# Kernel tuning notes

Measured on AMD Instinct MI355X. Metric: run time of the kernel, lower is better.

The kernel has to match this reference:

```python
import jax, jax.numpy as jnp
import numpy as np

B, SEQ, PRED, DM = 16, 2048, 2048, 64
P = SEQ + PRED            # PointNum = 4096, per-node feature length
NLAYER, HID = 3, 4096     # MLPNums, ggdmodel hidden sizes
NH, HS = 16, 4096         # NumAttentionHeads, HiddenSize
G_CONST, K = 1.0, 8
NN = DM * DM              # 4096 == P, MHSA input dim (required by original code)


def setup_inputs() -> dict:
    key = jax.random.key(0)
    ks = jax.random.split(key, 11)
    s_mlp = 1.0 / np.sqrt(P).astype(np.float32)
    s_att = 1.0 / np.sqrt(NN).astype(np.float32)
    s_out = 1.0 / np.sqrt(HS).astype(np.float32)
    return {
        "x": jax.random.normal(ks[0], (B, P, DM), jnp.float32),
        "W_mlp": jax.random.normal(ks[1], (NLAYER, P, HID), jnp.float32) * s_mlp,
        "b_mlp": jnp.zeros((NLAYER, HID), jnp.float32),
        "Wq": jax.random.normal(ks[2], (NN, HS), jnp.float32) * s_att,
        "bq": jnp.zeros((HS,), jnp.float32),
        "Wk": jax.random.normal(ks[3], (NN, HS), jnp.float32) * s_att,
        "bk": jnp.zeros((HS,), jnp.float32),
        "Wv": jax.random.normal(ks[4], (NN, HS), jnp.float32) * s_att,
        "bv": jnp.zeros((HS,), jnp.float32),
        "Wo": jax.random.normal(ks[5], (HS, HS), jnp.float32) * s_out,
        "bo": jnp.zeros((HS,), jnp.float32),
    }


def _grav_adj(h):
    # h: [B, N, D] node features -> symmetrized, top-K masked gravity adjacency [B, N, N]
    norm = jnp.linalg.norm(h, axis=-1)                      # [B, N]
    m = jnp.sum(h, axis=-1) / norm                          # node "mass"
    sim = jnp.einsum('bnd,bmd->bnm', h, h) / (norm[:, :, None] * norm[:, None, :])
    F = G_CONST * m[:, :, None] * m[:, None, :] * sim * sim  # gravity matrix
    kth = jax.lax.top_k(F, K)[0][..., -1:]                  # per-row Kth largest value
    F = jnp.where(F >= kth, F, 0.0)                         # keep only top-K per row
    F = jnp.maximum(F, 0.0)                                 # ReLU
    return 0.5 * (F + jnp.swapaxes(F, -1, -2))              # symmetrize


def reference(x, W_mlp, b_mlp, Wq, bq, Wk, bk, Wv, bv, Wo, bo):
    h = jnp.swapaxes(x, 1, 2)                               # [B, N=DM, P]
    adjs = [_grav_adj(h)]
    for l in range(NLAYER):                                 # each MLP applied to the same h
        hv = h @ W_mlp[l] + b_mlp[l]                        # [B, N, HID]
        adjs.append(_grav_adj(hv))
    A = jnp.stack(adjs, axis=1)                             # [B, L, N, N], L = NLAYER + 1
    Lseq = A.shape[1]
    tok = A.reshape(B, Lseq, NN)                            # L tokens of dim N*N
    dh = HS // NH
    q = (tok @ Wq + bq).reshape(B, Lseq, NH, dh)
    k = (tok @ Wk + bk).reshape(B, Lseq, NH, dh)
    v = (tok @ Wv + bv).reshape(B, Lseq, NH, dh)
    scores = jnp.einsum('blhd,bmhd->bhlm', q, k) / np.sqrt(dh).astype(np.float32)
    attn = jax.nn.softmax(scores, axis=-1)
    ctx = jnp.einsum('bhlm,bmhd->blhd', attn, v).reshape(B, Lseq, HS)
    out = ctx @ Wo + bo                                     # [B, L, HS]
    return jnp.where(out > 0.5, out, 0.0)
```

## Files before the change

### kernel.cpp

```cpp
#include <hip/hip_runtime.h>
#include <math.h>


#define B16 16
#define PDIM 4096
#define NNODE 64
#define NCHUNK 32
#define KCG 128

typedef __attribute__((ext_vector_type(8))) short bf16x8;
typedef __attribute__((ext_vector_type(4))) float f32x4;
typedef __attribute__((ext_vector_type(4))) unsigned short us4;
typedef __attribute__((ext_vector_type(8))) unsigned short us8;

__device__ inline void split2(float x, unsigned short& h, unsigned short& l) {
  unsigned u = __float_as_uint(x);
  unsigned hu = (u + 0x7fffu + ((u >> 16) & 1u)) & 0xffff0000u;
  h = (unsigned short)(hu >> 16);
  float lo = x - __uint_as_float(hu);
  unsigned u2 = __float_as_uint(lo);
  l = (unsigned short)((u2 + 0x7fffu + ((u2 >> 16) & 1u)) >> 16);
}

__device__ inline void gload16(const void* g, void* lds) {
  __builtin_amdgcn_global_load_lds((const unsigned int*)g, (unsigned int*)lds, 16, 0, 0);
}

__global__ __launch_bounds__(256) void k_transpose(const float* __restrict__ x,
                                                   float* __restrict__ h,
                                                   unsigned short* __restrict__ AhT,
                                                   unsigned short* __restrict__ AlT,
                                                   int mode) {
  __shared__ float t[64][65];
  int b = blockIdx.y;
  int p0 = blockIdx.x * 64;
  const float* xb = x + (size_t)b * PDIM * NNODE;
#pragma unroll
  for (int i = 0; i < 16; ++i) {
    int e = i * 256 + threadIdx.x;
    int p = e >> 6, n = e & 63;
    t[p][n] = xb[(size_t)p0 * 64 + e];
  }
  __syncthreads();
  if (mode != 2) {
    float* hb = h + (size_t)b * NNODE * PDIM;
#pragma unroll
    for (int i = 0; i < 16; ++i) {
      int e = i * 256 + threadIdx.x;
      int n = e >> 6, p = e & 63;
      hb[(size_t)n * PDIM + p0 + p] = t[p][n];
    }
  }
  if (mode == 0) return;
#pragma unroll
  for (int j = 0; j < 2; ++j) {
    int cid = j * 256 + threadIdx.x;
    int n2 = cid >> 3, kg8 = cid & 7;
    us8 hv_, lv_;
#pragma unroll
    for (int e = 0; e < 8; ++e) {
      unsigned short hh, ll;
      split2(t[kg8 * 8 + e][n2], hh, ll);
      hv_[e] = hh; lv_[e] = ll;
    }
    int m = b * 64 + n2;
    int ks = (p0 >> 5) + (kg8 >> 2);
    size_t idx = (((size_t)(m >> 7) * 128 + ks) * 8 + ((m >> 4) & 7)) * 512 +
                 (size_t)((n2 & 15) + 16 * (kg8 & 3)) * 8;
    *(us8*)&AhT[idx] = hv_;
    *(us8*)&AlT[idx] = lv_;
  }
}

__global__ __launch_bounds__(256) void k_wsplit(const float* __restrict__ W,
                                                unsigned short* __restrict__ WhT,
                                                unsigned short* __restrict__ WlT) {
  __shared__ float Wt[32][132];
  int nb = blockIdx.x, kb = blockIdx.y;
  int tid = threadIdx.x;
#pragma unroll
  for (int i = 0; i < 4; ++i) {
    int idx = i * 256 + tid;
    int row = idx >> 5, c4 = idx & 31;
    float4 v = *(const float4*)&W[(size_t)(kb * 32 + row) * 4096 + nb * 128 + c4 * 4];
    *(float4*)&Wt[row][c4 * 4] = v;
  }
  __syncthreads();
#pragma unroll
  for (int j = 0; j < 2; ++j) {
    int cid = j * 256 + tid;
    int nl = cid & 127, kg = cid >> 7;
    us8 hv_, lv_;
#pragma unroll
    for (int e = 0; e < 8; ++e) {
      unsigned short hh, ll;
      split2(Wt[kg * 8 + e][nl], hh, ll);
      hv_[e] = hh; lv_[e] = ll;
    }
    size_t idx = (((size_t)nb * 128 + kb) * 8 + (nl >> 4)) * 512 +
                 (size_t)((nl & 15) + 16 * kg) * 8;
    *(us8*)&WhT[idx] = hv_;
    *(us8*)&WlT[idx] = lv_;
  }
}

__global__ __launch_bounds__(1024) void k_gemm_mlp(
    const unsigned short* __restrict__ Ah, const unsigned short* __restrict__ Al,
    const unsigned short* __restrict__ Bh, const unsigned short* __restrict__ Bl,
    float* __restrict__ Cp) {
  __shared__ unsigned short sAh[2][8192], sAl[2][8192];
  __shared__ unsigned short sBh[2][8192], sBl[2][8192];
  int tid = threadIdx.x;
  int l = tid & 63, wid = tid >> 6;
  int wr = wid >> 2, wc = wid & 3;
  int nb = blockIdx.x, mb = blockIdx.y, z = blockIdx.z;
  const int spp = 32;
  int ks0 = z * spp;

  int half = tid >> 9, off8 = (tid & 511) * 8;
  size_t gA = (size_t)(mb * 2 + half) * 128;
  size_t gB = (size_t)(nb * 2 + half) * 128;

  f32x4 acc[4][4];
#pragma unroll
  for (int i = 0; i < 4; ++i)
#pragma unroll
    for (int j = 0; j < 4; ++j) acc[i][j] = (f32x4){0.f, 0.f, 0.f, 0.f};

  gload16(Ah + (gA + ks0) * 4096 + off8, &sAh[0][tid * 8]);
  gload16(Al + (gA + ks0) * 4096 + off8, &sAl[0][tid * 8]);
  gload16(Bh + (gB + ks0) * 4096 + off8, &sBh[0][tid * 8]);
  gload16(Bl + (gB + ks0) * 4096 + off8, &sBl[0][tid * 8]);
  __syncthreads();

  int buf = 0;
  for (int t = 0; t < spp; ++t) {
    if (t + 1 < spp) {
      size_t ks = ks0 + t + 1;
      gload16(Ah + (gA + ks) * 4096 + off8, &sAh[buf ^ 1][tid * 8]);
      gload16(Al + (gA + ks) * 4096 + off8, &sAl[buf ^ 1][tid * 8]);
      gload16(Bh + (gB + ks) * 4096 + off8, &sBh[buf ^ 1][tid * 8]);
      gload16(Bl + (gB + ks) * 4096 + off8, &sBl[buf ^ 1][tid * 8]);
    }
    bf16x8 ah[4], al4[4], bh4[4], bl4[4];
#pragma unroll
    for (int i = 0; i < 4; ++i) {
      ah[i]  = *(const bf16x8*)&sAh[buf][(wr * 4 + i) * 512 + l * 8];
      al4[i] = *(const bf16x8*)&sAl[buf][(wr * 4 + i) * 512 + l * 8];
      bh4[i] = *(const bf16x8*)&sBh[buf][(wc * 4 + i) * 512 + l * 8];
      bl4[i] = *(const bf16x8*)&sBl[buf][(wc * 4 + i) * 512 + l * 8];
    }
#pragma unroll
    for (int mt = 0; mt < 4; ++mt)
#pragma unroll
      for (int nt = 0; nt < 4; ++nt) {
        acc[mt][nt] = __builtin_amdgcn_mfma_f32_16x16x32_bf16(ah[mt],  bh4[nt], acc[mt][nt], 0, 0, 0);
        acc[mt][nt] = __builtin_amdgcn_mfma_f32_16x16x32_bf16(ah[mt],  bl4[nt], acc[mt][nt], 0, 0, 0);
        acc[mt][nt] = __builtin_amdgcn_mfma_f32_16x16x32_bf16(al4[mt], bh4[nt], acc[mt][nt], 0, 0, 0);
      }
    __syncthreads();
    buf ^= 1;
  }

  int n0 = nb * 256, m0 = mb * 256;
  float* Cz = Cp + (size_t)z * (1024 * 4096);
#pragma unroll
  for (int mt = 0; mt < 4; ++mt)
#pragma unroll
    for (int nt = 0; nt < 4; ++nt) {
      int col = n0 + wc * 64 + nt * 16 + (l & 15);
      int rowb = m0 + wr * 64 + mt * 16 + ((l >> 4) << 2);
#pragma unroll
      for (int r = 0; r < 4; ++r)
        Cz[(size_t)(rowb + r) * 4096 + col] = acc[mt][nt][r];
    }
}

__global__ __launch_bounds__(512) void k_gemm_wsf32(
    const unsigned short* __restrict__ Ah, const unsigned short* __restrict__ Al,
    const float* __restrict__ W0, const float* __restrict__ W1,
    const float* __restrict__ W2, float* __restrict__ Cp, int ksplit) {
  __shared__ unsigned short sAh[2][2048], sAl[2][2048];
  __shared__ unsigned short sBh[2][4096], sBl[2][4096];
  int tid = threadIdx.x;
  int l = tid & 63, wid = tid >> 6;
  int wr = wid >> 2, wc = wid & 3;
  int nb = blockIdx.x, z = blockIdx.z;
  int mat = z / ksplit, kz = z - mat * ksplit;
  const float* W = (mat == 0) ? W0 : ((mat == 1) ? W1 : W2);
  int nsteps = 128 / ksplit;
  int ks0 = kz * nsteps;
  int n0 = nb * 128;

  const float* wbase = W + (size_t)((l >> 4) * 8) * 4096 + n0 + wid * 16 + (l & 15);
  int sidx = wid * 512 + l * 8;

  f32x4 acc[2][2];
#pragma unroll
  for (int i = 0; i < 2; ++i)
#pragma unroll
    for (int j = 0; j < 2; ++j) acc[i][j] = (f32x4){0.f, 0.f, 0.f, 0.f};

  {
    if (tid < 256) gload16(Ah + (size_t)ks0 * 4096 + tid * 8, &sAh[0][tid * 8]);
    else           gload16(Al + (size_t)ks0 * 4096 + (tid - 256) * 8, &sAl[0][(tid - 256) * 8]);
    float wv[8];
#pragma unroll
    for (int e = 0; e < 8; ++e) wv[e] = wbase[(size_t)ks0 * 131072 + (size_t)e * 4096];
    us8 hi, lo;
#pragma unroll
    for (int e = 0; e < 8; ++e) {
      unsigned short hh, ll;
      split2(wv[e], hh, ll);
      hi[e] = hh; lo[e] = ll;
    }
    *(us8*)&sBh[0][sidx] = hi;
    *(us8*)&sBl[0][sidx] = lo;
  }
  __syncthreads();

  int buf = 0;
  for (int t = 0; t < nsteps; ++t) {
    bool more = (t + 1 < nsteps);
    float wv[8];
    if (more) {
      int ks = ks0 + t + 1;
      if (tid < 256) gload16(Ah + (size_t)ks * 4096 + tid * 8, &sAh[buf ^ 1][tid * 8]);
      else           gload16(Al + (size_t)ks * 4096 + (tid - 256) * 8, &sAl[buf ^ 1][(tid - 256) * 8]);
#pragma unroll
      for (int e = 0; e < 8; ++e) wv[e] = wbase[(size_t)ks * 131072 + (size_t)e * 4096];
    }
    bf16x8 aH[2], aL[2], bH[2], bL[2];
#pragma unroll
    for (int i = 0; i < 2; ++i) {
      aH[i] = *(const bf16x8*)&sAh[buf][(wr * 2 + i) * 512 + l * 8];
      aL[i] = *(const bf16x8*)&sAl[buf][(wr * 2 + i) * 512 + l * 8];
      bH[i] = *(const bf16x8*)&sBh[buf][(wc * 2 + i) * 512 + l * 8];
      bL[i] = *(const bf16x8*)&sBl[buf][(wc * 2 + i) * 512 + l * 8];
    }
#pragma unroll
    for (int i = 0; i < 2; ++i)
#pragma unroll
      for (int j = 0; j < 2; ++j) {
        acc[i][j] = __builtin_amdgcn_mfma_f32_16x16x32_bf16(aH[i], bH[j], acc[i][j], 0, 0, 0);
        acc[i][j] = __builtin_amdgcn_mfma_f32_16x16x32_bf16(aH[i], bL[j], acc[i][j], 0, 0, 0);
        acc[i][j] = __builtin_amdgcn_mfma_f32_16x16x32_bf16(aL[i], bH[j], acc[i][j], 0, 0, 0);
      }
    if (more) {
      us8 hi, lo;
#pragma unroll
      for (int e = 0; e < 8; ++e) {
        unsigned short hh, ll;
        split2(wv[e], hh, ll);
        hi[e] = hh; lo[e] = ll;
      }
      *(us8*)&sBh[buf ^ 1][sidx] = hi;
      *(us8*)&sBl[buf ^ 1][sidx] = lo;
    }
    __syncthreads();
    buf ^= 1;
  }

  float* Cz = Cp + (size_t)z * 262144;
#pragma unroll
  for (int i = 0; i < 2; ++i)
#pragma unroll
    for (int j = 0; j < 2; ++j) {
      int col = n0 + wc * 32 + j * 16 + (l & 15);
#pragma unroll
      for (int r = 0; r < 4; ++r) {
        int row = (wr * 2 + i) * 16 + ((l >> 4) << 2) + r;
        Cz[(size_t)row * 4096 + col] = acc[i][j][r];
      }
    }
}

__global__ __launch_bounds__(256) void k_red_mlp_split(const float* __restrict__ Cp,
                                                       const float* __restrict__ bias,
                                                       unsigned short* __restrict__ hvh,
                                                       unsigned short* __restrict__ hvl) {
  int c = blockIdx.x * 256 + threadIdx.x;
  int m = c >> 9, kc = c & 511;
  int k0 = kc * 8;
  const float* p = Cp + (size_t)m * 4096 + k0;
  us8 hv_, lv_;
#pragma unroll
  for (int e = 0; e < 8; ++e) {
    float v = p[e] + p[e + 4194304] + p[e + 2 * 4194304] + p[e + 3 * 4194304] + bias[k0 + e];
    unsigned short hh, ll;
    split2(v, hh, ll);
    hv_[e] = hh; lv_[e] = ll;
  }
  int batch = m >> 6, rr = m & 63;
  size_t idx = (size_t)batch * 262144 + (size_t)(kc >> 2) * 2048 +
               (size_t)(rr >> 4) * 512 + (size_t)((rr & 15) + 16 * (kc & 3)) * 8;
  *(us8*)&hvh[idx] = hv_;
  *(us8*)&hvl[idx] = lv_;
}

__global__ __launch_bounds__(256) void k_gram_mfma(
    const unsigned short* __restrict__ Zh, const unsigned short* __restrict__ Zl,
    float* __restrict__ Gp, float* __restrict__ Sp,
    int bs1, int ks_stride, int nsteps) {
  __shared__ unsigned short sZh[2][2048], sZl[2][2048];
  int z = blockIdx.x, b = blockIdx.y;
  int tid = threadIdx.x;
  int l = tid & 63, w = tid >> 6;
  size_t zbase = (size_t)(b >> 1) * 524288 + (size_t)(b & 1) * bs1;
  int ks0 = z * nsteps;

  f32x4 acc[4], racc;
#pragma unroll
  for (int j = 0; j < 4; ++j) acc[j] = (f32x4){0.f, 0.f, 0.f, 0.f};
  racc = (f32x4){0.f, 0.f, 0.f, 0.f};
  bf16x8 ones;
#pragma unroll
  for (int e = 0; e < 8; ++e) ones[e] = (short)0x3F80;

  gload16(Zh + zbase + (size_t)ks0 * ks_stride + tid * 8, &sZh[0][tid * 8]);
  gload16(Zl + zbase + (size_t)ks0 * ks_stride + tid * 8, &sZl[0][tid * 8]);
  __syncthreads();

  int buf = 0;
  for (int t = 0; t < nsteps; ++t) {
    if (t + 1 < nsteps) {
      size_t off = zbase + (size_t)(ks0 + t + 1) * ks_stride + tid * 8;
      gload16(Zh + off, &sZh[buf ^ 1][tid * 8]);
      gload16(Zl + off, &sZl[buf ^ 1][tid * 8]);
    }
    bf16x8 bh[4], bl4[4];
#pragma unroll
    for (int nt = 0; nt < 4; ++nt) {
      bh[nt]  = *(const bf16x8*)&sZh[buf][nt * 512 + l * 8];
      bl4[nt] = *(const bf16x8*)&sZl[buf][nt * 512 + l * 8];
    }
    bf16x8 ah = bh[w], al = bl4[w];
#pragma unroll
    for (int nt = 0; nt < 4; ++nt) {
      acc[nt] = __builtin_amdgcn_mfma_f32_16x16x32_bf16(ah, bh[nt], acc[nt], 0, 0, 0);
      acc[nt] = __builtin_amdgcn_mfma_f32_16x16x32_bf16(ah, bl4[nt], acc[nt], 0, 0, 0);
      acc[nt] = __builtin_amdgcn_mfma_f32_16x16x32_bf16(al, bh[nt], acc[nt], 0, 0, 0);
    }
    racc = __builtin_amdgcn_mfma_f32_16x16x32_bf16(ah, ones, racc, 0, 0, 0);
    racc = __builtin_amdgcn_mfma_f32_16x16x32_bf16(al, ones, racc, 0, 0, 0);
    __syncthreads();
    buf ^= 1;
  }

  float* Gz = Gp + ((size_t)z * B16 + b) * 4096;
#pragma unroll
  for (int nt = 0; nt < 4; ++nt) {
    int col = nt * 16 + (l & 15);
#pragma unroll
    for (int r = 0; r < 4; ++r) {
      int row = w * 16 + ((l >> 4) << 2) + r;
      Gz[row * 64 + col] = acc[nt][r];
    }
  }
  if ((l & 15) == 0) {
    float* Sz = Sp + ((size_t)z * B16 + b) * 64;
#pragma unroll
    for (int r = 0; r < 4; ++r) Sz[w * 16 + ((l >> 4) << 2) + r] = racc[r];
  }
}

__global__ __launch_bounds__(256) void k_gred8(const float* __restrict__ Gp,
                                               const float* __restrict__ Sp,
                                               float* __restrict__ G,
                                               float* __restrict__ S, int slot) {
  int idx = blockIdx.x * 256 + threadIdx.x;
  if (idx < 65536) {
    float s = 0.f;
#pragma unroll
    for (int c = 0; c < 8; ++c) s += Gp[(size_t)c * 65536 + idx];
    G[(size_t)slot * 65536 + idx] = s;
  } else if (idx < 66560) {
    int i2 = idx - 65536;
    float s = 0.f;
#pragma unroll
    for (int c = 0; c < 8; ++c) s += Sp[(size_t)c * 1024 + i2];
    S[(size_t)slot * 1024 + i2] = s;
  }
}

__global__ __launch_bounds__(256) void k_redqkv8(const float* __restrict__ Cp,
                                                 const float* __restrict__ bq,
                                                 const float* __restrict__ bk,
                                                 const float* __restrict__ bv,
                                                 float* __restrict__ q,
                                                 float* __restrict__ k,
                                                 float* __restrict__ v) {
  int idx = blockIdx.x * 256 + threadIdx.x;
  int mat = idx >> 18;
  int rn = idx & ((1 << 18) - 1);
  int n = rn & 4095;
  const float* base = Cp + (size_t)mat * 8 * 262144;
  float s = 0.f;
#pragma unroll
  for (int p = 0; p < 8; ++p) s += base[(size_t)p * 262144 + rn];
  if (mat == 0) q[rn] = s + bq[n];
  else if (mat == 1) k[rn] = s + bk[n];
  else v[rn] = s + bv[n];
}

__global__ __launch_bounds__(256) void k_redN(const float* __restrict__ Cp,
                                              const float* __restrict__ bias,
                                              float* __restrict__ dst,
                                              int nparts, int thr) {
  int idx = blockIdx.x * 256 + threadIdx.x;
  float s = bias[idx & 4095];
  for (int p = 0; p < nparts; ++p) s += Cp[(size_t)p * 262144 + idx];
  if (thr) s = (s > 0.5f) ? s : 0.f;
  dst[idx] = s;
}

__device__ inline float wmax64(float v) {
#pragma unroll
  for (int off = 32; off; off >>= 1) v = fmaxf(v, __shfl_xor(v, off));
  return v;
}

__global__ __launch_bounds__(256) void k_adj_t(const float* __restrict__ G,
                                               const float* __restrict__ S,
                                               unsigned short* __restrict__ tokh,
                                               unsigned short* __restrict__ tokl) {
  __shared__ float Fm[64][64];
  __shared__ float nrm[64], mm[64];
  int b = blockIdx.x >> 2, lz = blockIdx.x & 3;
  int tid = threadIdx.x;
  int j = tid & 63, w = tid >> 6;
  const float* Gb = G + ((size_t)lz * B16 + b) * 4096;
  const float* Sb = S + ((size_t)lz * B16 + b) * 64;
  if (tid < 64) {
    float nj = sqrtf(Gb[tid * 64 + tid]);
    nrm[tid] = nj;
    mm[tid] = Sb[tid] / nj;
  }
  __syncthreads();
  for (int i = w; i < 64; i += 4) {
    float g = Gb[i * 64 + j];
    float sim = g / (nrm[i] * nrm[j]);
    Fm[i][j] = mm[i] * mm[j] * sim * sim;
  }
  __syncthreads();
  for (int i = w; i < 64; i += 4) {
    float f = Fm[i][j];
    int cnt = 0;
#pragma unroll
    for (int u4 = 0; u4 < 16; ++u4) {
      float4 q = *(const float4*)&Fm[i][u4 * 4];
      cnt += (q.x > f) + (q.y > f) + (q.z > f) + (q.w > f);
    }
    float cand = (cnt <= 7) ? f : INFINITY;
#pragma unroll
    for (int off = 32; off; off >>= 1) cand = fminf(cand, __shfl_xor(cand, off));
    float fm = (f >= cand) ? fmaxf(f, 0.f) : 0.f;
    Fm[i][j] = fm;
  }
  __syncthreads();
  int r = b * 4 + lz;
  int mt = r >> 4, rl = r & 15;
#pragma unroll
  for (int c = 0; c < 2; ++c) {
    int cid = tid * 2 + c;
    int jj0 = cid >> 3, g = cid & 7;
    us8 hv_, lv_;
#pragma unroll
    for (int e = 0; e < 8; ++e) {
      int kcol = g * 8 + e;
      float val = 0.5f * (Fm[jj0][kcol] + Fm[kcol][jj0]);
      unsigned short hh, ll;
      split2(val, hh, ll);
      hv_[e] = hh; lv_[e] = ll;
    }
    int ks = jj0 * 2 + (g >> 2);
    size_t idx = ((size_t)ks * 8 + mt) * 512 + (size_t)(rl + 16 * (g & 3)) * 8;
    *(us8*)&tokh[idx] = hv_;
    *(us8*)&tokl[idx] = lv_;
  }
}

__global__ __launch_bounds__(64) void k_attn_t(const float* __restrict__ q,
                                               const float* __restrict__ k,
                                               const float* __restrict__ v,
                                               unsigned short* __restrict__ ctxh,
                                               unsigned short* __restrict__ ctxl) {
  __shared__ float cb[4][256];
  int hd = blockIdx.x, b = blockIdx.y;
  int t = threadIdx.x;
  float qr[4][4], kr[4][4], vr[4][4];
#pragma unroll
  for (int l = 0; l < 4; ++l)
#pragma unroll
    for (int s = 0; s < 4; ++s) {
      size_t off = ((size_t)(b * 4 + l)) * 4096 + hd * 256 + t + s * 64;
      qr[l][s] = q[off]; kr[l][s] = k[off]; vr[l][s] = v[off];
    }
  float sc[4][4];
#pragma unroll
  for (int l = 0; l < 4; ++l)
#pragma unroll
    for (int m = 0; m < 4; ++m) {
      float p = 0.f;
#pragma unroll
      for (int s = 0; s < 4; ++s) p = fmaf(qr[l][s], kr[m][s], p);
#pragma unroll
      for (int off = 32; off; off >>= 1) p += __shfl_xor(p, off);
      sc[l][m] = p * (1.0f / 16.0f);
    }
  float at[4][4];
#pragma unroll
  for (int l = 0; l < 4; ++l) {
    float mx = fmaxf(fmaxf(sc[l][0], sc[l][1]), fmaxf(sc[l][2], sc[l][3]));
    float e0 = expf(sc[l][0] - mx), e1 = expf(sc[l][1] - mx);
    float e2 = expf(sc[l][2] - mx), e3 = expf(sc[l][3] - mx);
    float d = e0 + e1 + e2 + e3;
    at[l][0] = e0 / d; at[l][1] = e1 / d; at[l][2] = e2 / d; at[l][3] = e3 / d;
  }
#pragma unroll
  for (int l = 0; l < 4; ++l)
#pragma unroll
    for (int s = 0; s < 4; ++s) {
      float c = 0.f;
#pragma unroll
      for (int m = 0; m < 4; ++m) c = fmaf(at[l][m], vr[m][s], c);
      cb[l][s * 64 + t] = c;
    }
  __syncthreads();
  int lq = t >> 4, c16 = t & 15;
  int mt = b >> 2, rl = (b & 3) * 4 + lq;
#pragma unroll
  for (int e8 = 0; e8 < 2; ++e8) {
    us8 hv_, lv_;
#pragma unroll
    for (int e = 0; e < 8; ++e) {
      unsigned short hh, ll;
      split2(cb[lq][c16 * 16 + e8 * 8 + e], hh, ll);
      hv_[e] = hh; lv_[e] = ll;
    }
    int ks = hd * 8 + (c16 >> 1);
    size_t idx = ((size_t)ks * 8 + mt) * 512 + (size_t)(rl + 16 * ((c16 * 2 + e8) & 3)) * 8;
    *(us8*)&ctxh[idx] = hv_;
    *(us8*)&ctxl[idx] = lv_;
  }
}

__global__ __launch_bounds__(256) void k_gram_partial(const float* __restrict__ Z,
                                                      float* __restrict__ Gp,
                                                      float* __restrict__ Sp) {
  __shared__ float Zt[KCG][68];
  int c = blockIdx.x, b = blockIdx.y;
  int tid = threadIdx.x;
  const float* Zb = Z + (size_t)b * NNODE * PDIM + c * KCG;
#pragma unroll
  for (int i = 0; i < 32; ++i) {
    int e = i * 256 + tid;
    int r = e >> 7, kk = e & 127;
    Zt[kk][r] = Zb[(size_t)r * PDIM + kk];
  }
  __syncthreads();
  int ii = tid >> 2, j0 = (tid & 3) << 4;
  float acc[16] = {};
  for (int kk = 0; kk < KCG; ++kk) {
    float zi = Zt[kk][ii];
    float4 z0 = *(const float4*)&Zt[kk][j0 + 0];
    float4 z1 = *(const float4*)&Zt[kk][j0 + 4];
    float4 z2 = *(const float4*)&Zt[kk][j0 + 8];
    float4 z3 = *(const float4*)&Zt[kk][j0 + 12];
    acc[0] = fmaf(zi, z0.x, acc[0]);   acc[1] = fmaf(zi, z0.y, acc[1]);
    acc[2] = fmaf(zi, z0.z, acc[2]);   acc[3] = fmaf(zi, z0.w, acc[3]);
    acc[4] = fmaf(zi, z1.x, acc[4]);   acc[5] = fmaf(zi, z1.y, acc[5]);
    acc[6] = fmaf(zi, z1.z, acc[6]);   acc[7] = fmaf(zi, z1.w, acc[7]);
    acc[8] = fmaf(zi, z2.x, acc[8]);   acc[9] = fmaf(zi, z2.y, acc[9]);
    acc[10] = fmaf(zi, z2.z, acc[10]); acc[11] = fmaf(zi, z2.w, acc[11]);
    acc[12] = fmaf(zi, z3.x, acc[12]); acc[13] = fmaf(zi, z3.y, acc[13]);
    acc[14] = fmaf(zi, z3.z, acc[14]); acc[15] = fmaf(zi, z3.w, acc[15]);
  }
  float* gp = Gp + ((size_t)c * B16 + b) * 4096 + ii * 64 + j0;
#pragma unroll
  for (int j = 0; j < 16; ++j) gp[j] = acc[j];
  if (tid < 64) {
    float s = 0.f;
    for (int kk = 0; kk < KCG; ++kk) s += Zt[kk][tid];
    Sp[((size_t)c * B16 + b) * 64 + tid] = s;
  }
}

__global__ __launch_bounds__(256) void k_gram_reduce(const float* __restrict__ Gp,
                                                     const float* __restrict__ Sp,
                                                     float* __restrict__ G,
                                                     float* __restrict__ S, int slot) {
  int idx = blockIdx.x * 256 + threadIdx.x;
  if (idx < B16 * 4096) {
    float s = 0.f;
    for (int c = 0; c < NCHUNK; ++c) s += Gp[(size_t)c * (B16 * 4096) + idx];
    G[(size_t)slot * (B16 * 4096) + idx] = s;
  } else {
    int idx2 = idx - B16 * 4096;
    float s = 0.f;
    for (int c = 0; c < NCHUNK; ++c) s += Sp[(size_t)c * (B16 * 64) + idx2];
    S[(size_t)slot * (B16 * 64) + idx2] = s;
  }
}

__global__ __launch_bounds__(256) void k_gemm_mfma(
    const float* __restrict__ A, const float* __restrict__ B0,
    const float* __restrict__ B1, const float* __restrict__ B2,
    const float* __restrict__ bias, float* __restrict__ C,
    int mrows, int mstore, int N, int K, int ksplit) {
  __shared__ __align__(16) unsigned short sA[2][8][64][8];
  __shared__ __align__(16) unsigned short sB[2][8][64][8];
  int z = blockIdx.z;
  int mat = z / ksplit, ks = z - mat * ksplit;
  const float* Bm = (mat == 0) ? B0 : ((mat == 1) ? B1 : B2);
  int kchunk = K / ksplit;
  int k0 = ks * kchunk, k1 = k0 + kchunk;
  int tid = threadIdx.x;
  int l = tid & 63;
  int wr = (tid >> 7) & 1, wc = (tid >> 6) & 1;
  int m0 = blockIdx.y * 128, n0g = blockIdx.x * 128;
  bool activeM = (m0 + wr * 64) < mstore;
  int am = tid >> 1;
  int arow = m0 + am; if (arow >= mrows) arow = mrows - 1;
  const float* Arow = A + (size_t)arow * K;
  int amt = am >> 4;
  int bk = tid >> 3;
  int bnb = (tid & 7) * 4;
  int bg = bk >> 3, bslot = bk & 7;
  f32x4 acc[4][4];
#pragma unroll
  for (int i = 0; i < 4; ++i)
#pragma unroll
    for (int j = 0; j < 4; ++j) acc[i][j] = (f32x4){0.f, 0.f, 0.f, 0.f};
  for (int kb = k0; kb < k1; kb += 32) {
    __syncthreads();
#pragma unroll
    for (int i = 0; i < 4; ++i) {
      int kq = (tid & 1) * 4 + i * 8;
      float4 a = *(const float4*)(Arow + kb + kq);
      unsigned short h0, h1, h2, h3, l0, l1, l2, l3;
      split2(a.x, h0, l0); split2(a.y, h1, l1);
      split2(a.z, h2, l2); split2(a.w, h3, l3);
      int lane_t = (am & 15) + 16 * (kq >> 3);
      int sb = kq & 4;
      *(us4*)&sA[0][amt][lane_t][sb] = (us4){h0, h1, h2, h3};
      *(us4*)&sA[1][amt][lane_t][sb] = (us4){l0, l1, l2, l3};
    }
    {
      const float* Brow = Bm + (size_t)(kb + bk) * N + n0g;
#pragma unroll
      for (int i = 0; i < 4; ++i) {
        int n = bnb + i * 32;
        int nt = n >> 4, nr = n & 15;
        float4 b = *(const float4*)(Brow + n);
        float be[4] = {b.x, b.y, b.z, b.w};
#pragma unroll
        for (int e = 0; e < 4; ++e) {
          unsigned short hh, ll;
          split2(be[e], hh, ll);
          sB[0][nt][nr + e + 16 * bg][bslot] = hh;
          sB[1][nt][nr + e + 16 * bg][bslot] = ll;
        }
      }
    }
    __syncthreads();
    if (!activeM) continue;
    bf16x8 ah[4], al[4], bh[4], bl[4];
#pragma unroll
    for (int t = 0; t < 4; ++t) {
      ah[t] = *(const bf16x8*)&sA[0][wr * 4 + t][l][0];
      al[t] = *(const bf16x8*)&sA[1][wr * 4 + t][l][0];
      bh[t] = *(const bf16x8*)&sB[0][wc * 4 + t][l][0];
      bl[t] = *(const bf16x8*)&sB[1][wc * 4 + t][l][0];
    }
#pragma unroll
    for (int mt = 0; mt < 4; ++mt)
#pragma unroll
      for (int nt = 0; nt < 4; ++nt) {
        acc[mt][nt] = __builtin_amdgcn_mfma_f32_16x16x32_bf16(ah[mt], bh[nt], acc[mt][nt], 0, 0, 0);
        acc[mt][nt] = __builtin_amdgcn_mfma_f32_16x16x32_bf16(ah[mt], bl[nt], acc[mt][nt], 0, 0, 0);
        acc[mt][nt] = __builtin_amdgcn_mfma_f32_16x16x32_bf16(al[mt], bh[nt], acc[mt][nt], 0, 0, 0);
      }
  }
  if (!activeM) return;
  float* Cz = C + (size_t)z * mstore * N;
#pragma unroll
  for (int mt = 0; mt < 4; ++mt)
#pragma unroll
    for (int nt = 0; nt < 4; ++nt) {
      int col = n0g + wc * 64 + nt * 16 + (l & 15);
      float badd = bias ? bias[col] : 0.f;
#pragma unroll
      for (int r = 0; r < 4; ++r) {
        int row = m0 + wr * 64 + mt * 16 + ((l >> 4) << 2) + r;
        if (row < mstore) Cz[(size_t)row * N + col] = acc[mt][nt][r] + badd;
      }
    }
}

__global__ __launch_bounds__(64) void k_adj_fb(const float* __restrict__ G,
                                               const float* __restrict__ S,
                                               float* __restrict__ tok) {
  __shared__ float Fm[64][64];
  __shared__ float nrm[64], mm[64];
  int b = blockIdx.x >> 2, lz = blockIdx.x & 3;
  int j = threadIdx.x;
  const float* Gb = G + ((size_t)lz * B16 + b) * 4096;
  const float* Sb = S + ((size_t)lz * B16 + b) * 64;
  float nj = sqrtf(Gb[j * 64 + j]);
  nrm[j] = nj;
  mm[j] = Sb[j] / nj;
  __syncthreads();
  for (int i = 0; i < 64; ++i) {
    float g = Gb[i * 64 + j];
    float sim = g / (nrm[i] * nj);
    float F = mm[i] * mm[j] * sim * sim;
    float v = F;
    bool act = true;
    float kth = 0.f;
#pragma unroll
    for (int it = 0; it < 8; ++it) {
      float mv = wmax64(act ? v : -INFINITY);
      kth = mv;
      unsigned long long ball = __ballot(act && (v == mv));
      int first = __ffsll(ball) - 1;
      if (j == first) act = false;
    }
    float fm = (F >= kth) ? F : 0.f;
    Fm[i][j] = fmaxf(fm, 0.f);
  }
  __syncthreads();
  float* tb = tok + ((size_t)b * 4 + lz) * 4096;
  for (int i = 0; i < 64; ++i) tb[i * 64 + j] = 0.5f * (Fm[i][j] + Fm[j][i]);
}

__global__ __launch_bounds__(256) void k_qkv_reduce(const float* __restrict__ Cp,
                                                    const float* __restrict__ bq,
                                                    const float* __restrict__ bk,
                                                    const float* __restrict__ bv,
                                                    float* __restrict__ q,
                                                    float* __restrict__ k,
                                                    float* __restrict__ v) {
  int idx = blockIdx.x * 256 + threadIdx.x;
  int mat = idx >> 18;
  int rn = idx & ((1 << 18) - 1);
  int n = rn & 4095;
  const float* base = Cp + (size_t)mat * 4 * 262144;
  float s = base[rn] + base[rn + 262144] + base[rn + 2 * 262144] + base[rn + 3 * 262144];
  if (mat == 0) q[rn] = s + bq[n];
  else if (mat == 1) k[rn] = s + bk[n];
  else v[rn] = s + bv[n];
}

__global__ __launch_bounds__(64) void k_attn_fb(const float* __restrict__ q,
                                                const float* __restrict__ k,
                                                const float* __restrict__ v,
                                                float* __restrict__ ctx) {
  int hd = blockIdx.x, b = blockIdx.y;
  int t = threadIdx.x;
  float qr[4][4], kr[4][4], vr[4][4];
#pragma unroll
  for (int l = 0; l < 4; ++l)
#pragma unroll
    for (int s = 0; s < 4; ++s) {
      size_t off = ((size_t)(b * 4 + l)) * 4096 + hd * 256 + t + s * 64;
      qr[l][s] = q[off]; kr[l][s] = k[off]; vr[l][s] = v[off];
    }
  float sc[4][4];
#pragma unroll
  for (int l = 0; l < 4; ++l)
#pragma unroll
    for (int m = 0; m < 4; ++m) {
      float p = 0.f;
#pragma unroll
      for (int s = 0; s < 4; ++s) p = fmaf(qr[l][s], kr[m][s], p);
#pragma unroll
      for (int off = 32; off; off >>= 1) p += __shfl_xor(p, off);
      sc[l][m] = p * (1.0f / 16.0f);
    }
  float at[4][4];
#pragma unroll
  for (int l = 0; l < 4; ++l) {
    float mx = fmaxf(fmaxf(sc[l][0], sc[l][1]), fmaxf(sc[l][2], sc[l][3]));
    float e0 = expf(sc[l][0] - mx), e1 = expf(sc[l][1] - mx);
    float e2 = expf(sc[l][2] - mx), e3 = expf(sc[l][3] - mx);
    float d = e0 + e1 + e2 + e3;
    at[l][0] = e0 / d; at[l][1] = e1 / d; at[l][2] = e2 / d; at[l][3] = e3 / d;
  }
#pragma unroll
  for (int l = 0; l < 4; ++l)
#pragma unroll
    for (int s = 0; s < 4; ++s) {
      float c = 0.f;
#pragma unroll
      for (int m = 0; m < 4; ++m) c = fmaf(at[l][m], vr[m][s], c);
      ctx[((size_t)(b * 4 + l)) * 4096 + hd * 256 + t + s * 64] = c;
    }
}

__global__ __launch_bounds__(256) void k_out_reduce(const float* __restrict__ Cp,
                                                    const float* __restrict__ bo,
                                                    float* __restrict__ out) {
  int idx = blockIdx.x * 256 + threadIdx.x;
  int n = idx & 4095;
  float s = bo[n];
#pragma unroll
  for (int p = 0; p < 8; ++p) s += Cp[(size_t)p * 262144 + idx];
  out[idx] = (s > 0.5f) ? s : 0.f;
}

extern "C" void kernel_launch(void* const* d_in, const int* in_sizes, int n_in,
                              void* d_out, int out_size, void* d_ws, size_t ws_size,
                              hipStream_t stream) {
  const float* x     = (const float*)d_in[0];
  const float* W_mlp = (const float*)d_in[1];
  const float* b_mlp = (const float*)d_in[2];
  const float* Wq = (const float*)d_in[3]; const float* bq = (const float*)d_in[4];
  const float* Wk = (const float*)d_in[5]; const float* bk = (const float*)d_in[6];
  const float* Wv = (const float*)d_in[7]; const float* bv = (const float*)d_in[8];
  const float* Wo = (const float*)d_in[9]; const float* bo = (const float*)d_in[10];
  float* out = (float*)d_out;
  float* ws = (float*)d_ws;

  float* h   = ws;
  float* Gp  = ws + 8388608;
  float* Sp  = ws + 10485760;
  float* G   = ws + 10518528;
  float* S   = ws + 10780672;

  const size_t NEED = 50368512ull * 4ull;
  if (ws_size >= NEED) {
    unsigned short* hvh = (unsigned short*)(ws + 4194304);
    unsigned short* hvl = (unsigned short*)(ws + 6291456);
    float* q   = ws + 10784768;
    float* kk  = ws + 11046912;
    float* vv  = ws + 11309056;
    unsigned short* AhT = (unsigned short*)(ws + 11571200);
    unsigned short* AlT = (unsigned short*)(ws + 13668352);
    unsigned short* WhT = (unsigned short*)(ws + 15765504);
    unsigned short* WlT = (unsigned short*)(ws + 24154112);
    float* Cp           = ws + 32542720;
    unsigned short* tokh = (unsigned short*)(ws + 49319936);
    unsigned short* tokl = (unsigned short*)(ws + 49582080);
    unsigned short* ctxh = (unsigned short*)(ws + 49844224);
    unsigned short* ctxl = (unsigned short*)(ws + 50106368);

    k_transpose<<<dim3(64, 16), 256, 0, stream>>>(x, h, AhT, AlT, 2);

    k_gram_mfma<<<dim3(8, 16), 256, 0, stream>>>(AhT, AlT, Gp, Sp, 2048, 4096, 16);
    k_gred8<<<260, 256, 0, stream>>>(Gp, Sp, G, S, 0);

    for (int l = 0; l < 3; ++l) {
      k_wsplit<<<dim3(32, 128), 256, 0, stream>>>(W_mlp + (size_t)l * 16777216, WhT, WlT);
      k_gemm_mlp<<<dim3(16, 4, 4), 1024, 0, stream>>>(AhT, AlT, WhT, WlT, Cp);
      k_red_mlp_split<<<2048, 256, 0, stream>>>(Cp, b_mlp + (size_t)l * 4096, hvh, hvl);
      k_gram_mfma<<<dim3(8, 16), 256, 0, stream>>>(hvh, hvl, Gp, Sp, 262144, 2048, 16);
      k_gred8<<<260, 256, 0, stream>>>(Gp, Sp, G, S, l + 1);
    }

    k_adj_t<<<64, 256, 0, stream>>>(G, S, tokh, tokl);

    k_gemm_wsf32<<<dim3(32, 1, 24), 512, 0, stream>>>(tokh, tokl, Wq, Wk, Wv, Cp, 8);
    k_redqkv8<<<3072, 256, 0, stream>>>(Cp, bq, bk, bv, q, kk, vv);

    k_attn_t<<<dim3(16, 16), 64, 0, stream>>>(q, kk, vv, ctxh, ctxl);

    k_gemm_wsf32<<<dim3(32, 1, 8), 512, 0, stream>>>(ctxh, ctxl, Wo, Wo, Wo, Cp, 8);
    k_redN<<<1024, 256, 0, stream>>>(Cp, bo, out, 8, 1);
  } else {
    float* hv  = ws + 4194304;
    float* tok = ws + 10784768;
    float* q   = ws + 11046912;
    float* kk  = ws + 11309056;
    float* vv  = ws + 11571200;
    float* ctx = ws + 11833344;
    float* qkvp = hv;
    float* op   = h;

    k_transpose<<<dim3(64, 16), 256, 0, stream>>>(x, h, (unsigned short*)0,
                                                  (unsigned short*)0, 0);
    k_gram_partial<<<dim3(NCHUNK, 16), 256, 0, stream>>>(h, Gp, Sp);
    k_gram_reduce<<<260, 256, 0, stream>>>(Gp, Sp, G, S, 0);
    for (int l = 0; l < 3; ++l) {
      const float* Wl = W_mlp + (size_t)l * PDIM * 4096;
      const float* bl = b_mlp + (size_t)l * 4096;
      k_gemm_mfma<<<dim3(32, 8, 1), 256, 0, stream>>>(h, Wl, Wl, Wl, bl, hv,
                                                      1024, 1024, 4096, 4096, 1);
      k_gram_partial<<<dim3(NCHUNK, 16), 256, 0, stream>>>(hv, Gp, Sp);
      k_gram_reduce<<<260, 256, 0, stream>>>(Gp, Sp, G, S, l + 1);
    }
    k_adj_fb<<<64, 64, 0, stream>>>(G, S, tok);
    k_gemm_mfma<<<dim3(32, 1, 12), 256, 0, stream>>>(tok, Wq, Wk, Wv, nullptr, qkvp,
                                                     64, 64, 4096, 4096, 4);
    k_qkv_reduce<<<3072, 256, 0, stream>>>(qkvp, bq, bk, bv, q, kk, vv);
    k_attn_fb<<<dim3(16, 16), 64, 0, stream>>>(q, kk, vv, ctx);
    k_gemm_mfma<<<dim3(32, 1, 8), 256, 0, stream>>>(ctx, Wo, Wo, Wo, nullptr, op,
                                                    64, 64, 4096, 4096, 8);
    k_out_reduce<<<1024, 256, 0, stream>>>(op, bo, out);
  }
}
```

Measured before the change: 654.8 us.

## Prefetch two stages ahead in split-bf16 GEMM with fine-grained vmcnt waits

Restructures the double-buffered LDS pipeline of the split-bf16 GEMM. Both buffers are now loaded up front, and each iteration issues the load for stage t+2 after the compute barrier. Explicit s_waitcnt vmcnt(4) plus raw s_barrier replace __syncthreads, so one stage of async global-to-LDS loads stays in flight during the MFMA work. This is meant to hide global load latency better. It relies on the direct-to-LDS loads being counted by vmcnt and correctly ordered, and any mistake there risks a race.

```diff
diff --git a/kernel.cpp b/kernel.cpp
--- a/kernel.cpp
+++ b/kernel.cpp
@@ -127,21 +127,22 @@
 #pragma unroll
     for (int j = 0; j < 4; ++j) acc[i][j] = (f32x4){0.f, 0.f, 0.f, 0.f};
 
-  gload16(Ah + (gA + ks0) * 4096 + off8, &sAh[0][tid * 8]);
-  gload16(Al + (gA + ks0) * 4096 + off8, &sAl[0][tid * 8]);
-  gload16(Bh + (gB + ks0) * 4096 + off8, &sBh[0][tid * 8]);
-  gload16(Bl + (gB + ks0) * 4096 + off8, &sBl[0][tid * 8]);
-  __syncthreads();
-
-  int buf = 0;
+  gload16(Ah + (gA + ks0 + 0) * 4096 + off8, &sAh[0][tid * 8]);
+  gload16(Al + (gA + ks0 + 0) * 4096 + off8, &sAl[0][tid * 8]);
+  gload16(Bh + (gB + ks0 + 0) * 4096 + off8, &sBh[0][tid * 8]);
+  gload16(Bl + (gB + ks0 + 0) * 4096 + off8, &sBl[0][tid * 8]);
+  gload16(Ah + (gA + ks0 + 1) * 4096 + off8, &sAh[1][tid * 8]);
+  gload16(Al + (gA + ks0 + 1) * 4096 + off8, &sAl[1][tid * 8]);
+  gload16(Bh + (gB + ks0 + 1) * 4096 + off8, &sBh[1][tid * 8]);
+  gload16(Bl + (gB + ks0 + 1) * 4096 + off8, &sBl[1][tid * 8]);
+
   for (int t = 0; t < spp; ++t) {
-    if (t + 1 < spp) {
-      size_t ks = ks0 + t + 1;
-      gload16(Ah + (gA + ks) * 4096 + off8, &sAh[buf ^ 1][tid * 8]);
-      gload16(Al + (gA + ks) * 4096 + off8, &sAl[buf ^ 1][tid * 8]);
-      gload16(Bh + (gB + ks) * 4096 + off8, &sBh[buf ^ 1][tid * 8]);
-      gload16(Bl + (gB + ks) * 4096 + off8, &sBl[buf ^ 1][tid * 8]);
-    }
+    int buf = t & 1;
+    if (t + 1 < spp) asm volatile("s_waitcnt vmcnt(4)" ::: "memory");
+    else             asm volatile("s_waitcnt vmcnt(0)" ::: "memory");
+    __builtin_amdgcn_s_barrier();
+    asm volatile("" ::: "memory");
+
     bf16x8 ah[4], al4[4], bh4[4], bl4[4];
 #pragma unroll
     for (int i = 0; i < 4; ++i) {
@@ -158,8 +159,17 @@
         acc[mt][nt] = __builtin_amdgcn_mfma_f32_16x16x32_bf16(ah[mt],  bl4[nt], acc[mt][nt], 0, 0, 0);
         acc[mt][nt] = __builtin_amdgcn_mfma_f32_16x16x32_bf16(al4[mt], bh4[nt], acc[mt][nt], 0, 0, 0);
       }
-    __syncthreads();
-    buf ^= 1;
+
+    asm volatile("" ::: "memory");
+    __builtin_amdgcn_s_barrier();
+    asm volatile("" ::: "memory");
+    if (t + 2 < spp) {
+      size_t ks = ks0 + t + 2;
+      gload16(Ah + (gA + ks) * 4096 + off8, &sAh[buf][tid * 8]);
+      gload16(Al + (gA + ks) * 4096 + off8, &sAl[buf][tid * 8]);
+      gload16(Bh + (gB + ks) * 4096 + off8, &sBh[buf][tid * 8]);
+      gload16(Bl + (gB + ks) * 4096 + off8, &sBl[buf][tid * 8]);
+    }
   }
 
   int n0 = nb * 256, m0 = mb * 256;
```

Result: no change. 647.3 us (-1.2%).

## Fuse weight bf16 split into MLP GEMM and partial-sum reduction into Gram kernel

Applied to the files above, without the earlier changes.

Removes the separate weight-splitting pass by loading fp32 MLP weights directly in the GEMM and splitting them into hi/lo bf16 in registers before writing to LDS. It also drops the reduce-and-split kernel: the Gram kernel now sums the split-K partials, adds the bias, splits into hi/lo and computes row sums with a ones-vector MFMA. The GEMM tiling changes to 512 threads, 128-row tiles and split-K of 2. This cuts extra global round trips and kernel launches. The cost is uncoalesced strided fp32 weight loads and split arithmetic inside the GEMM main loop.

```diff
diff --git a/kernel.cpp b/kernel.cpp
--- a/kernel.cpp
+++ b/kernel.cpp
@@ -72,54 +72,28 @@
   }
 }
 
-__global__ __launch_bounds__(256) void k_wsplit(const float* __restrict__ W,
-                                                unsigned short* __restrict__ WhT,
-                                                unsigned short* __restrict__ WlT) {
-  __shared__ float Wt[32][132];
-  int nb = blockIdx.x, kb = blockIdx.y;
-  int tid = threadIdx.x;
-#pragma unroll
-  for (int i = 0; i < 4; ++i) {
-    int idx = i * 256 + tid;
-    int row = idx >> 5, c4 = idx & 31;
-    float4 v = *(const float4*)&W[(size_t)(kb * 32 + row) * 4096 + nb * 128 + c4 * 4];
-    *(float4*)&Wt[row][c4 * 4] = v;
-  }
-  __syncthreads();
-#pragma unroll
-  for (int j = 0; j < 2; ++j) {
-    int cid = j * 256 + tid;
-    int nl = cid & 127, kg = cid >> 7;
-    us8 hv_, lv_;
-#pragma unroll
-    for (int e = 0; e < 8; ++e) {
-      unsigned short hh, ll;
-      split2(Wt[kg * 8 + e][nl], hh, ll);
-      hv_[e] = hh; lv_[e] = ll;
-    }
-    size_t idx = (((size_t)nb * 128 + kb) * 8 + (nl >> 4)) * 512 +
-                 (size_t)((nl & 15) + 16 * kg) * 8;
-    *(us8*)&WhT[idx] = hv_;
-    *(us8*)&WlT[idx] = lv_;
-  }
-}
-
-__global__ __launch_bounds__(1024) void k_gemm_mlp(
+__global__ __launch_bounds__(512) void k_gemm_mlpf(
     const unsigned short* __restrict__ Ah, const unsigned short* __restrict__ Al,
-    const unsigned short* __restrict__ Bh, const unsigned short* __restrict__ Bl,
-    float* __restrict__ Cp) {
-  __shared__ unsigned short sAh[2][8192], sAl[2][8192];
+    const float* __restrict__ W, float* __restrict__ Cp) {
+  __shared__ unsigned short sAh[2][4096], sAl[2][4096];
   __shared__ unsigned short sBh[2][8192], sBl[2][8192];
   int tid = threadIdx.x;
   int l = tid & 63, wid = tid >> 6;
   int wr = wid >> 2, wc = wid & 3;
   int nb = blockIdx.x, mb = blockIdx.y, z = blockIdx.z;
-  const int spp = 32;
+  const int spp = 64;
   int ks0 = z * spp;
 
-  int half = tid >> 9, off8 = (tid & 511) * 8;
-  size_t gA = (size_t)(mb * 2 + half) * 128;
-  size_t gB = (size_t)(nb * 2 + half) * 128;
+  size_t abase = ((size_t)mb * 128 + ks0) * 4096 + tid * 8;
+
+  const float* wb[2];
+  int sidx[2];
+#pragma unroll
+  for (int c = 0; c < 2; ++c) {
+    int tc = wid + 8 * c;
+    wb[c] = W + (size_t)((l >> 4) * 8) * 4096 + nb * 256 + tc * 16 + (l & 15);
+    sidx[c] = tc * 512 + l * 8;
+  }
 
   f32x4 acc[4][4];
 #pragma unroll
@@ -127,20 +101,35 @@
 #pragma unroll
     for (int j = 0; j < 4; ++j) acc[i][j] = (f32x4){0.f, 0.f, 0.f, 0.f};
 
-  gload16(Ah + (gA + ks0) * 4096 + off8, &sAh[0][tid * 8]);
-  gload16(Al + (gA + ks0) * 4096 + off8, &sAl[0][tid * 8]);
-  gload16(Bh + (gB + ks0) * 4096 + off8, &sBh[0][tid * 8]);
-  gload16(Bl + (gB + ks0) * 4096 + off8, &sBl[0][tid * 8]);
+  gload16(Ah + abase, &sAh[0][tid * 8]);
+  gload16(Al + abase, &sAl[0][tid * 8]);
+#pragma unroll
+  for (int c = 0; c < 2; ++c) {
+    us8 hi, lo;
+#pragma unroll
+    for (int e = 0; e < 8; ++e) {
+      unsigned short hh, ll;
+      split2(wb[c][(size_t)ks0 * 131072 + (size_t)e * 4096], hh, ll);
+      hi[e] = hh; lo[e] = ll;
+    }
+    *(us8*)&sBh[0][sidx[c]] = hi;
+    *(us8*)&sBl[0][sidx[c]] = lo;
+  }
   __syncthreads();
 
   int buf = 0;
   for (int t = 0; t < spp; ++t) {
-    if (t + 1 < spp) {
-      size_t ks = ks0 + t + 1;
-      gload16(Ah + (gA + ks) * 4096 + off8, &sAh[buf ^ 1][tid * 8]);
-      gload16(Al + (gA + ks) * 4096 + off8, &sAl[buf ^ 1][tid * 8]);
-      gload16(Bh + (gB + ks) * 4096 + off8, &sBh[buf ^ 1][tid * 8]);
-      gload16(Bl + (gB + ks) * 4096 + off8, &sBl[buf ^ 1][tid * 8]);
+    bool more = (t + 1 < spp);
+    float wv[2][8];
+    if (more) {
+      size_t off = abase + (size_t)(t + 1) * 4096;
+      gload16(Ah + off, &sAh[buf ^ 1][tid * 8]);
+      gload16(Al + off, &sAl[buf ^ 1][tid * 8]);
+      size_t wo = (size_t)(ks0 + t + 1) * 131072;
+#pragma unroll
+      for (int c = 0; c < 2; ++c)
+#pragma unroll
+        for (int e = 0; e < 8; ++e) wv[c][e] = wb[c][wo + (size_t)e * 4096];
     }
     bf16x8 ah[4], al4[4], bh4[4], bl4[4];
 #pragma unroll
@@ -158,12 +147,26 @@
         acc[mt][nt] = __builtin_amdgcn_mfma_f32_16x16x32_bf16(ah[mt],  bl4[nt], acc[mt][nt], 0, 0, 0);
         acc[mt][nt] = __builtin_amdgcn_mfma_f32_16x16x32_bf16(al4[mt], bh4[nt], acc[mt][nt], 0, 0, 0);
       }
+    if (more) {
+#pragma unroll
+      for (int c = 0; c < 2; ++c) {
+        us8 hi, lo;
+#pragma unroll
+        for (int e = 0; e < 8; ++e) {
+          unsigned short hh, ll;
+          split2(wv[c][e], hh, ll);
+          hi[e] = hh; lo[e] = ll;
+        }
+        *(us8*)&sBh[buf ^ 1][sidx[c]] = hi;
+        *(us8*)&sBl[buf ^ 1][sidx[c]] = lo;
+      }
+    }
     __syncthreads();
     buf ^= 1;
   }
 
-  int n0 = nb * 256, m0 = mb * 256;
-  float* Cz = Cp + (size_t)z * (1024 * 4096);
+  int n0 = nb * 256, m0 = mb * 128;
+  float* Cz = Cp + (size_t)z * 4194304;
 #pragma unroll
   for (int mt = 0; mt < 4; ++mt)
 #pragma unroll
@@ -275,27 +278,80 @@
     }
 }
 
-__global__ __launch_bounds__(256) void k_red_mlp_split(const float* __restrict__ Cp,
-                                                       const float* __restrict__ bias,
-                                                       unsigned short* __restrict__ hvh,
-                                                       unsigned short* __restrict__ hvl) {
-  int c = blockIdx.x * 256 + threadIdx.x;
-  int m = c >> 9, kc = c & 511;
-  int k0 = kc * 8;
-  const float* p = Cp + (size_t)m * 4096 + k0;
-  us8 hv_, lv_;
-#pragma unroll
-  for (int e = 0; e < 8; ++e) {
-    float v = p[e] + p[e + 4194304] + p[e + 2 * 4194304] + p[e + 3 * 4194304] + bias[k0 + e];
-    unsigned short hh, ll;
-    split2(v, hh, ll);
-    hv_[e] = hh; lv_[e] = ll;
-  }
-  int batch = m >> 6, rr = m & 63;
-  size_t idx = (size_t)batch * 262144 + (size_t)(kc >> 2) * 2048 +
-               (size_t)(rr >> 4) * 512 + (size_t)((rr & 15) + 16 * (kc & 3)) * 8;
-  *(us8*)&hvh[idx] = hv_;
-  *(us8*)&hvl[idx] = lv_;
+__global__ __launch_bounds__(256) void k_gram_fuse(
+    const float* __restrict__ Cp, const float* __restrict__ bias,
+    float* __restrict__ Gp, float* __restrict__ Sp, int nparts) {
+  __shared__ unsigned short sZh[2048], sZl[2048];
+  int zk = blockIdx.x, b = blockIdx.y;
+  int tid = threadIdx.x;
+  int l = tid & 63, w = tid >> 6;
+  int srow = tid >> 2, skq = tid & 3;
+  const float* cbase = Cp + (size_t)(b * 64 + srow) * 4096;
+  int swidx = (srow >> 4) * 512 + (skq * 16 + (srow & 15)) * 8;
+
+  f32x4 acc[4], racc;
+#pragma unroll
+  for (int j = 0; j < 4; ++j) acc[j] = (f32x4){0.f, 0.f, 0.f, 0.f};
+  racc = (f32x4){0.f, 0.f, 0.f, 0.f};
+  bf16x8 ones;
+#pragma unroll
+  for (int e = 0; e < 8; ++e) ones[e] = (short)0x3F80;
+
+  for (int s = 0; s < 8; ++s) {
+    int k0 = zk * 256 + s * 32 + skq * 8;
+    float v[8];
+#pragma unroll
+    for (int e = 0; e < 8; ++e) v[e] = bias[k0 + e];
+    for (int p = 0; p < nparts; ++p) {
+      const float* pp = cbase + (size_t)p * 4194304 + k0;
+      float4 a0 = *(const float4*)pp;
+      float4 a1 = *(const float4*)(pp + 4);
+      v[0] += a0.x; v[1] += a0.y; v[2] += a0.z; v[3] += a0.w;
+      v[4] += a1.x; v[5] += a1.y; v[6] += a1.z; v[7] += a1.w;
+    }
+    us8 hi, lo;
+#pragma unroll
+    for (int e = 0; e < 8; ++e) {
+      unsigned short hh, ll;
+      split2(v[e], hh, ll);
+      hi[e] = hh; lo[e] = ll;
+    }
+    *(us8*)&sZh[swidx] = hi;
+    *(us8*)&sZl[swidx] = lo;
+    __syncthreads();
+    bf16x8 bh[4], bl4[4];
+#pragma unroll
+    for (int nt = 0; nt < 4; ++nt) {
+      bh[nt]  = *(const bf16x8*)&sZh[nt * 512 + l * 8];
+      bl4[nt] = *(const bf16x8*)&sZl[nt * 512 + l * 8];
+    }
+    bf16x8 ah = bh[w], al = bl4[w];
+#pragma unroll
+    for (int nt = 0; nt < 4; ++nt) {
+      acc[nt] = __builtin_amdgcn_mfma_f32_16x16x32_bf16(ah, bh[nt], acc[nt], 0, 0, 0);
+      acc[nt] = __builtin_amdgcn_mfma_f32_16x16x32_bf16(ah, bl4[nt], acc[nt], 0, 0, 0);
+      acc[nt] = __builtin_amdgcn_mfma_f32_16x16x32_bf16(al, bh[nt], acc[nt], 0, 0, 0);
+    }
+    racc = __builtin_amdgcn_mfma_f32_16x16x32_bf16(ah, ones, racc, 0, 0, 0);
+    racc = __builtin_amdgcn_mfma_f32_16x16x32_bf16(al, ones, racc, 0, 0, 0);
+    __syncthreads();
+  }
+
+  float* Gz = Gp + ((size_t)zk * B16 + b) * 4096;
+#pragma unroll
+  for (int nt = 0; nt < 4; ++nt) {
+    int col = nt * 16 + (l & 15);
+#pragma unroll
+    for (int r = 0; r < 4; ++r) {
+      int row = w * 16 + ((l >> 4) << 2) + r;
+      Gz[row * 64 + col] = acc[nt][r];
+    }
+  }
+  if ((l & 15) == 0) {
+    float* Sz = Sp + ((size_t)zk * B16 + b) * 64;
+#pragma unroll
+    for (int r = 0; r < 4; ++r) Sz[w * 16 + ((l >> 4) << 2) + r] = racc[r];
+  }
 }
 
 __global__ __launch_bounds__(256) void k_gram_mfma(
@@ -364,21 +420,19 @@
   }
 }
 
-__global__ __launch_bounds__(256) void k_gred8(const float* __restrict__ Gp,
-                                               const float* __restrict__ Sp,
-                                               float* __restrict__ G,
-                                               float* __restrict__ S, int slot) {
+__global__ __launch_bounds__(256) void k_gred(const float* __restrict__ Gp,
+                                              const float* __restrict__ Sp,
+                                              float* __restrict__ G,
+                                              float* __restrict__ S, int slot, int nc) {
   int idx = blockIdx.x * 256 + threadIdx.x;
   if (idx < 65536) {
     float s = 0.f;
-#pragma unroll
-    for (int c = 0; c < 8; ++c) s += Gp[(size_t)c * 65536 + idx];
+    for (int c = 0; c < nc; ++c) s += Gp[(size_t)c * 65536 + idx];
     G[(size_t)slot * 65536 + idx] = s;
   } else if (idx < 66560) {
     int i2 = idx - 65536;
     float s = 0.f;
-#pragma unroll
-    for (int c = 0; c < 8; ++c) s += Sp[(size_t)c * 1024 + i2];
+    for (int c = 0; c < nc; ++c) s += Sp[(size_t)c * 1024 + i2];
     S[(size_t)slot * 1024 + i2] = s;
   }
 }
@@ -830,15 +884,11 @@
 
   const size_t NEED = 50368512ull * 4ull;
   if (ws_size >= NEED) {
-    unsigned short* hvh = (unsigned short*)(ws + 4194304);
-    unsigned short* hvl = (unsigned short*)(ws + 6291456);
     float* q   = ws + 10784768;
     float* kk  = ws + 11046912;
     float* vv  = ws + 11309056;
     unsigned short* AhT = (unsigned short*)(ws + 11571200);
     unsigned short* AlT = (unsigned short*)(ws + 13668352);
-    unsigned short* WhT = (unsigned short*)(ws + 15765504);
-    unsigned short* WlT = (unsigned short*)(ws + 24154112);
     float* Cp           = ws + 32542720;
     unsigned short* tokh = (unsigned short*)(ws + 49319936);
     unsigned short* tokl = (unsigned short*)(ws + 49582080);
@@ -848,14 +898,14 @@
     k_transpose<<<dim3(64, 16), 256, 0, stream>>>(x, h, AhT, AlT, 2);
 
     k_gram_mfma<<<dim3(8, 16), 256, 0, stream>>>(AhT, AlT, Gp, Sp, 2048, 4096, 16);
-    k_gred8<<<260, 256, 0, stream>>>(Gp, Sp, G, S, 0);
+    k_gred<<<260, 256, 0, stream>>>(Gp, Sp, G, S, 0, 8);
 
     for (int l = 0; l < 3; ++l) {
-      k_wsplit<<<dim3(32, 128), 256, 0, stream>>>(W_mlp + (size_t)l * 16777216, WhT, WlT);
-      k_gemm_mlp<<<dim3(16, 4, 4), 1024, 0, stream>>>(AhT, AlT, WhT, WlT, Cp);
-      k_red_mlp_split<<<2048, 256, 0, stream>>>(Cp, b_mlp + (size_t)l * 4096, hvh, hvl);
-      k_gram_mfma<<<dim3(8, 16), 256, 0, stream>>>(hvh, hvl, Gp, Sp, 262144, 2048, 16);
-      k_gred8<<<260, 256, 0, stream>>>(Gp, Sp, G, S, l + 1);
+      k_gemm_mlpf<<<dim3(16, 8, 2), 512, 0, stream>>>(AhT, AlT,
+                                                      W_mlp + (size_t)l * 16777216, Cp);
+      k_gram_fuse<<<dim3(16, 16), 256, 0, stream>>>(Cp, b_mlp + (size_t)l * 4096,
+                                                    Gp, Sp, 2);
+      k_gred<<<260, 256, 0, stream>>>(Gp, Sp, G, S, l + 1, 16);
     }
 
     k_adj_t<<<64, 256, 0, stream>>>(G, S, tokh, tokl);
```

After: 664.8 us. Within noise of the previous version (+1.5%).
